# Kernel tuning notes

Measured on AMD Instinct MI355X. Metric: run time of the kernel, lower is better.

Reference implementation:

```python
import math
import jax, jax.numpy as jnp
import numpy as np

B, T, FDIM, ODIM = 16, 16, 64, 8
NQ, LAYERS, DEGREE = 10, 2, 3
NA = 4                      # ceil(log2(T))
TOT = NQ + NA               # 14 total wires
NROTS = 4 * NQ * LAYERS     # 80 params per timestep
QROTS = 4 * NQ              # 40 (qff circuit, 1 layer)
C64 = jnp.complex64


def ry_mat(t):
    c = jnp.cos(0.5 * t).astype(C64)
    s = jnp.sin(0.5 * t).astype(C64)
    return jnp.stack([jnp.stack([c, -s], -1), jnp.stack([s, c], -1)], -2)


def rz_mat(t):
    p = jnp.exp(-0.5j * t.astype(C64))
    q = jnp.exp(0.5j * t.astype(C64))
    z = jnp.zeros_like(p)
    return jnp.stack([jnp.stack([p, z], -1), jnp.stack([z, q], -1)], -2)


def crx_mat(t):
    c = jnp.cos(0.5 * t).astype(C64)
    s = (-1j) * jnp.sin(0.5 * t).astype(C64)
    z = jnp.zeros_like(c)
    o = jnp.ones_like(c)
    r0 = jnp.stack([o, z, z, z], -1)
    r1 = jnp.stack([z, o, z, z], -1)
    r2 = jnp.stack([z, z, c, s], -1)
    r3 = jnp.stack([z, z, s, c], -1)
    return jnp.stack([r0, r1, r2, r3], -2)


CNOT = jnp.array([[1, 0, 0, 0], [0, 1, 0, 0], [0, 0, 0, 1], [0, 0, 1, 0]], dtype=C64)


def apply_gate(state, U, wires):
    # state: (Be, 2,...,2) tensor; wire w lives on axis w+1. U: (2^k,2^k) or (Be,2^k,2^k)
    k = len(wires)
    axes = [w + 1 for w in wires]
    st = jnp.moveaxis(state, axes, list(range(1, k + 1)))
    shp = st.shape
    st = st.reshape(shp[0], 2 ** k, -1)
    eq = 'bij,bjr->bir' if U.ndim == 3 else 'ij,bjr->bir'
    st = jnp.einsum(eq, U, st).reshape(shp)
    return jnp.moveaxis(st, list(range(1, k + 1)), axes)


def sim14_seq(nq, layers):
    # gate sequence of Sim et al. circuit 14: RY ring, CRX ring, RY ring, CRX counter-ring
    seq, idx = [], 0
    for _ in range(layers):
        for i in range(nq):
            seq.append(('ry', (i,), idx)); idx += 1
        for i in range(nq - 1, -1, -1):
            seq.append(('crx', (i, (i + 1) % nq), idx)); idx += 1
        for i in range(nq):
            seq.append(('ry', (i,), idx)); idx += 1
        for i in [nq - 1] + list(range(nq - 1)):
            seq.append(('crx', (i, (i - 1) % nq), idx)); idx += 1
    return seq


def apply_sim14(state, params, layers, adjoint=False):
    seq = sim14_seq(NQ, layers)
    if adjoint:
        seq = seq[::-1]
    sign = -1.0 if adjoint else 1.0
    for kind, w, pidx in seq:
        th = sign * params[..., pidx]
        U = ry_mat(th) if kind == 'ry' else crx_mat(th)
        state = apply_gate(state, U, list(w))
    return state


def apply_prepare(state, prep_p, adjoint=False):
    # learnable PREPARE ansatz on ancilla wires NQ..NQ+NA-1 (n_prep_layers == NA)
    seq = []
    for ly in range(NA):
        for qi in range(NA):
            seq.append(('ry', NQ + qi, (ly, qi, 0)))
            seq.append(('rz', NQ + qi, (ly, qi, 1)))
        for i in range(NA - 1):
            seq.append(('cnot', (NQ + i, NQ + i + 1), None))
    if adjoint:
        seq = seq[::-1]
    sign = -1.0 if adjoint else 1.0
    for kind, w, pix in seq:
        if kind == 'cnot':
            state = apply_gate(state, CNOT, list(w))
        else:
            th = sign * prep_p[pix]
            U = ry_mat(th) if kind == 'ry' else rz_mat(th)
            state = apply_gate(state, U, [w])
    return state


def pcphase(state, phi):
    # PennyLane PCPhase(phi, dim=2^NQ, wires=anc+main): e^{+i phi} on ancilla==0 subspace, e^{-i phi} elsewhere
    st = state.reshape(B, 2 ** NQ, 2 ** NA)
    ph = jnp.exp(1j * phi.astype(C64))
    vec = jnp.where(jnp.arange(2 ** NA) == 0, ph, jnp.conj(ph))
    return (st * vec).reshape((B,) + (2,) * TOT)


def apply_select(state, ts_params, adjoint=False):
    # Select: apply sim14(ts_params[:, j]) on main wires when ancilla register == j
    # (T == 2^NA so there is no identity padding). Vectorized over batch x ancilla index.
    st = state.reshape(B, 2 ** NQ, 2 ** NA)
    st = jnp.moveaxis(st, 2, 1).reshape((B * T,) + (2,) * NQ)
    st = apply_sim14(st, ts_params.reshape(B * T, NROTS), LAYERS, adjoint)
    st = st.reshape(B, 2 ** NA, 2 ** NQ)
    return jnp.moveaxis(st, 1, 2).reshape((B,) + (2,) * TOT)


def expvals(state):
    # <X_i>, <Y_i>, <Z_i> on main wires, order X0..X9, Y0..Y9, Z0..Z9
    xs, ys, zs = [], [], []
    for i in range(NQ):
        s = jnp.moveaxis(state, i + 1, 1).reshape(B, 2, -1)
        s0, s1 = s[:, 0], s[:, 1]
        c = jnp.sum(jnp.conj(s0) * s1, axis=-1)
        xs.append(2.0 * jnp.real(c))
        ys.append(2.0 * jnp.imag(c))
        zs.append(jnp.sum(jnp.abs(s0) ** 2 - jnp.abs(s1) ** 2, axis=-1))
    return jnp.stack(xs + ys + zs, axis=1).astype(jnp.float32)  # (B, 3*NQ)


def make_pe():
    pos = np.arange(T, dtype=np.float32)[:, None]
    div = np.exp(np.arange(0, FDIM, 2, dtype=np.float32) * -(math.log(10000.0) / FDIM))
    pe = np.zeros((T, FDIM), np.float32)
    pe[:, 0::2] = np.sin(pos * div)
    pe[:, 1::2] = np.cos(pos * div[:FDIM // 2])
    return jnp.asarray(pe)


def setup_inputs():
    key = jax.random.key(0)
    ks = jax.random.split(key, 8)
    return {
        'x': jax.random.normal(ks[0], (B, FDIM, T), jnp.float32),
        'W_fp': jax.random.normal(ks[1], (NROTS, FDIM), jnp.float32) / math.sqrt(FDIM),
        'b_fp': jnp.zeros((NROTS,), jnp.float32),
        'prep_p': 0.1 * jax.random.normal(ks[2], (NA, NA, 2), jnp.float32),
        'sig_ang': 0.1 * jax.random.normal(ks[3], (DEGREE + 1,), jnp.float32),
        'qff_p': jax.random.uniform(ks[4], (QROTS,), jnp.float32),
        'W_out': jax.random.normal(ks[5], (ODIM, 3 * NQ), jnp.float32) / math.sqrt(3 * NQ),
        'b_out': jnp.zeros((ODIM,), jnp.float32),
    }


def reference(x, W_fp, b_fp, prep_p, sig_ang, qff_p, W_out, b_out):
    h = jnp.transpose(x, (0, 2, 1)) + make_pe()[None]          # (B, T, FDIM)
    ts = jax.nn.sigmoid(h @ W_fp.T + b_fp) * (2.0 * math.pi)    # (B, T, NROTS)
    # |0...0> on all 14 wires, batched
    psi = jnp.zeros((B, 2 ** TOT), C64).at[:, 0].set(1.0).reshape((B,) + (2,) * TOT)
    psi = pcphase(psi, sig_ang[0])
    for k in range(DEGREE):
        psi = apply_prepare(psi, prep_p, adjoint=False)
        psi = apply_select(psi, ts, adjoint=(k % 2 == 1))
        psi = apply_prepare(psi, prep_p, adjoint=True)
        psi = pcphase(psi, sig_ang[k + 1])
    psi = apply_sim14(psi, qff_p, layers=1, adjoint=False)      # QFF readout circuit
    exps = expvals(psi)                                         # (B, 30)
    return exps @ W_out.T + b_out                               # (B, ODIM)
```

## Files before the change

kernel.cpp:

```cpp
#include <hip/hip_runtime.h>
#include <math.h>
#include <utility>


typedef float v2f __attribute__((ext_vector_type(2)));

struct Gate { int ry; int tbit; int cbit; int pidx; };
struct GateTab { Gate g[40]; };

constexpr GateTab make_gates1() {
  GateTab tb{};
  int pos = 0, idx = 0;
  for (int i = 0; i < 10; ++i) { tb.g[pos] = Gate{1, 9 - i, -1, idx}; ++pos; ++idx; }
  for (int i = 9; i >= 0; --i) { tb.g[pos] = Gate{0, 9 - ((i + 1) % 10), 9 - i, idx}; ++pos; ++idx; }
  for (int i = 0; i < 10; ++i) { tb.g[pos] = Gate{1, 9 - i, -1, idx}; ++pos; ++idx; }
  for (int k = 0; k < 10; ++k) {
    int i = (k == 0) ? 9 : (k - 1);
    tb.g[pos] = Gate{0, 9 - ((i + 9) % 10), 9 - i, idx}; ++pos; ++idx;
  }
  return tb;
}
constexpr GateTab GTC = make_gates1();

__device__ __forceinline__ int insert_zero(int v, int p) {
  return ((v >> p) << (p + 1)) | (v & ((1 << p) - 1));
}
__device__ __forceinline__ float2 cmul(float2 A, float2 B) {
  return make_float2(A.x * B.x - A.y * B.y, A.x * B.y + A.y * B.x);
}
__device__ __forceinline__ float2 conj2(float2 A) { return make_float2(A.x, -A.y); }
__device__ __forceinline__ v2f vmk(float x, float y) { v2f r; r.x = x; r.y = y; return r; }

template<int XM>
__device__ __forceinline__ float lxor(float v) {
  if constexpr (XM == 1) {
    int r = __builtin_amdgcn_update_dpp(__float_as_int(v), __float_as_int(v),
                                        0xB1, 0xF, 0xF, true);
    return __int_as_float(r);
  } else if constexpr (XM == 2) {
    int r = __builtin_amdgcn_update_dpp(__float_as_int(v), __float_as_int(v),
                                        0x4E, 0xF, 0xF, true);
    return __int_as_float(r);
  } else if constexpr (XM == 8) {
    int r = __builtin_amdgcn_update_dpp(__float_as_int(v), __float_as_int(v),
                                        0x128, 0xF, 0xF, true);
    return __int_as_float(r);
  } else if constexpr (XM == 16) {
#if __has_builtin(__builtin_amdgcn_permlane16_swap)
    unsigned uv = __float_as_uint(v);
    auto r = __builtin_amdgcn_permlane16_swap(uv, uv, false, false);
    return __uint_as_float(r[0] ^ r[1] ^ uv);
#else
    return __shfl_xor(v, 16, 64);
#endif
  } else if constexpr (XM == 32) {
#if __has_builtin(__builtin_amdgcn_permlane32_swap)
    unsigned uv = __float_as_uint(v);
    auto r = __builtin_amdgcn_permlane32_swap(uv, uv, false, false);
    return __uint_as_float(r[0] ^ r[1] ^ uv);
#else
    return __shfl_xor(v, 32, 64);
#endif
  } else {
    return __shfl_xor(v, XM, 64);
  }
}
template<int XM>
__device__ __forceinline__ v2f lxor2(v2f v) {
  v2f r; r.x = lxor<XM>(v.x); r.y = lxor<XM>(v.y); return r;
}

__device__ __forceinline__ float wave_sum(float v) {
  v += lxor<1>(v);
  v += lxor<2>(v);
  v += lxor<4>(v);
  v += lxor<8>(v);
  v += lxor<16>(v);
  v += lxor<32>(v);
  return v;
}

struct alignas(128) GBar {
  unsigned cnt;
  unsigned gen;
  unsigned done;
  unsigned pad[29];
};
__device__ GBar g_gb[16];

__device__ __forceinline__ void group_barrier16(int b, int lane) {
  unsigned snap = __hip_atomic_load(&g_gb[b].gen, __ATOMIC_RELAXED, __HIP_MEMORY_SCOPE_AGENT);
  if (lane == 0) {
    unsigned old = __hip_atomic_fetch_add(&g_gb[b].cnt, 1u, __ATOMIC_ACQ_REL,
                                          __HIP_MEMORY_SCOPE_AGENT);
    if ((old & 15u) == 15u)
      __hip_atomic_store(&g_gb[b].gen, snap + 1u, __ATOMIC_RELEASE,
                         __HIP_MEMORY_SCOPE_AGENT);
  }
  while (__hip_atomic_load(&g_gb[b].gen, __ATOMIC_RELAXED, __HIP_MEMORY_SCOPE_AGENT) == snap)
    __builtin_amdgcn_s_sleep(1);
  (void)__hip_atomic_load(&g_gb[b].gen, __ATOMIC_ACQUIRE, __HIP_MEMORY_SCOPE_AGENT);
}

template<int P>
__device__ __forceinline__ void ry_gate(v2f (&a)[16], float c, float s, int lane) {
  if constexpr (P < 4) {
    constexpr int m = 1 << P;
#pragma unroll
    for (int r0 = 0; r0 < 16; ++r0) {
      if (!(r0 & m)) {
        int r1 = r0 | m;
        v2f a0 = a[r0], a1 = a[r1];
        a[r0] = c * a0 - s * a1;
        a[r1] = s * a0 + c * a1;
      }
    }
  } else {
    constexpr int xm = 1 << (P - 4);
    bool up = (lane >> (P - 4)) & 1;
    float sg = up ? s : -s;
#pragma unroll
    for (int r = 0; r < 16; ++r) {
      v2f wv = lxor2<xm>(a[r]);
      a[r] = c * a[r] + sg * wv;
    }
  }
}

template<int P, int Q>
__device__ __forceinline__ void crx_gate(v2f (&a)[16], float c, float s, int lane) {
  if constexpr (P < 4) {
    constexpr int m = 1 << P;
#pragma unroll
    for (int r0 = 0; r0 < 16; ++r0) {
      if (!(r0 & m)) {
        int r1 = r0 | m;
        bool act;
        if constexpr (Q < 4) act = (r0 >> Q) & 1;
        else act = (lane >> (Q - 4)) & 1;
        if (act) {
          v2f a0 = a[r0], a1 = a[r1];
          a[r0] = c * a0 + s * vmk(a1.y, -a1.x);
          a[r1] = c * a1 + s * vmk(a0.y, -a0.x);
        }
      }
    }
  } else {
    constexpr int xm = 1 << (P - 4);
#pragma unroll
    for (int r = 0; r < 16; ++r) {
      v2f wv = lxor2<xm>(a[r]);
      bool act;
      if constexpr (Q < 4) act = (r >> Q) & 1;
      else act = (lane >> (Q - 4)) & 1;
      if (act) a[r] = c * a[r] + s * vmk(wv.y, -wv.x);
    }
  }
}

template<bool ADJ, int G>
__device__ __forceinline__ void one_gate(v2f (&a)[16], const float2 (&sc)[40], int lane) {
  constexpr Gate g = GTC.g[ADJ ? (39 - G) : G];
  float2 scv = sc[g.pidx];
  float s = ADJ ? -scv.x : scv.x;
  float c = scv.y;
  if constexpr (g.ry != 0) ry_gate<g.tbit>(a, c, s, lane);
  else crx_gate<g.tbit, g.cbit>(a, c, s, lane);
}

template<bool ADJ, int... I>
__device__ __forceinline__ void run_layer_impl(v2f (&a)[16], const float2 (&sc)[40],
                                               int lane, std::integer_sequence<int, I...>) {
  (one_gate<ADJ, I>(a, sc, lane), ...);
}

template<bool ADJ>
__device__ __forceinline__ void run_layer(v2f (&a)[16], const float2* sc, int lane) {
  float2 rsc[40];
#pragma unroll
  for (int i = 0; i < 40; ++i) rsc[i] = sc[i];
  run_layer_impl<ADJ>(a, rsc, lane, std::make_integer_sequence<int, 40>{});
}

__global__ __launch_bounds__(256, 1) void k_fused(const float* __restrict__ x,
                                                  const float* __restrict__ W_fp,
                                                  const float* __restrict__ b_fp,
                                                  const float* __restrict__ prep,
                                                  const float* __restrict__ sig,
                                                  const float* __restrict__ qff,
                                                  const float* __restrict__ W_out,
                                                  const float* __restrict__ b_out,
                                                  float* __restrict__ out,
                                                  float4* __restrict__ part1,
                                                  float4* __restrict__ part2,
                                                  float* __restrict__ sv) {
  int blk = blockIdx.x;
  int b = blk >> 2, sub = blk & 3;
  int tid = threadIdx.x;
  int w = tid >> 6, lane = tid & 63;
  int aa = sub * 4 + w;

  __shared__ __align__(16) float h[4][64];
  __shared__ float2 scs[4][80];
  __shared__ float2 qscs[40];
  __shared__ float2 ps[32];
  __shared__ float2 es[4];
  __shared__ float2 u0s[16];
  __shared__ float4 R[2][512];

  if (sub == 0 && w == 0 && lane < 30) sv[b * 30 + lane] = 0.f;

  {
    int f = lane, k = f >> 1;
    float div = expf(-(float)(2 * k) * (logf(10000.f) / 64.f));
    float ang = (float)aa * div;
    float pe = (f & 1) ? cosf(ang) : sinf(ang);
    h[w][f] = x[(b * 64 + f) * 16 + aa] + pe;
  }
  if (w == 0) {
    if (lane < 32) {
      float s, c;
      sincosf(0.5f * prep[lane], &s, &c);
      ps[lane] = make_float2(s, c);
    } else if (lane < 36) {
      float s, c;
      sincosf(sig[lane - 32], &s, &c);
      es[lane - 32] = make_float2(c, s);
    }
  } else if (w == 1 && lane < 40) {
    float s, c;
    sincosf(0.5f * qff[lane], &s, &c);
    qscs[lane] = make_float2(s, c);
  }
  __syncthreads();

  if (w == 0) {
    float2 v[16];
#pragma unroll
    for (int i = 0; i < 16; ++i) v[i] = make_float2(i == 0 ? 1.f : 0.f, 0.f);
#pragma unroll 1
    for (int ly = 0; ly < 4; ++ly) {
#pragma unroll
      for (int qi = 0; qi < 4; ++qi) {
        int p = 3 - qi;
        float2 rc = ps[ly * 8 + qi * 2 + 0];
        {
          float s = rc.x, c = rc.y;
#pragma unroll
          for (int m = 0; m < 8; ++m) {
            int a0 = insert_zero(m, p), a1 = a0 | (1 << p);
            float2 t0 = v[a0], t1 = v[a1];
            v[a0] = make_float2(c * t0.x - s * t1.x, c * t0.y - s * t1.y);
            v[a1] = make_float2(s * t0.x + c * t1.x, s * t0.y + c * t1.y);
          }
        }
        rc = ps[ly * 8 + qi * 2 + 1];
        {
          float s = rc.x, c = rc.y;
#pragma unroll
          for (int m = 0; m < 8; ++m) {
            int a0 = insert_zero(m, p), a1 = a0 | (1 << p);
            float2 t0 = v[a0], t1 = v[a1];
            v[a0] = make_float2(c * t0.x + s * t0.y, c * t0.y - s * t0.x);
            v[a1] = make_float2(c * t1.x - s * t1.y, c * t1.y + s * t1.x);
          }
        }
      }
#pragma unroll
      for (int i = 0; i < 3; ++i) {
        int pc = 3 - i, pt = 2 - i;
#pragma unroll
        for (int m = 0; m < 4; ++m) {
          int mm = insert_zero(m, pt);
          mm = insert_zero(mm, pc);
          int a0 = mm | (1 << pc), a1 = a0 | (1 << pt);
          float2 t0 = v[a0], t1 = v[a1];
          v[a0] = t1; v[a1] = t0;
        }
      }
    }
    if (lane == 0) {
#pragma unroll
      for (int i = 0; i < 16; ++i) u0s[i] = v[i];
    }
  }

  {
    const float4* h4 = (const float4*)&h[w][0];
    for (int j = lane; j < 80; j += 64) {
      float acc = b_fp[j];
      const float4* w4 = (const float4*)(W_fp + j * 64);
#pragma unroll
      for (int k4 = 0; k4 < 16; ++k4) {
        float4 hh = h4[k4], ww = w4[k4];
        acc += hh.x * ww.x + hh.y * ww.y + hh.z * ww.z + hh.w * ww.w;
      }
      float sg = 1.f / (1.f + expf(-acc));
      float s, c;
      sincosf(sg * 3.14159265358979323846f, &s, &c);
      scs[w][j] = make_float2(s, c);
    }
  }
  __syncthreads();

  float2 u0aa = u0s[aa];
  float2 e0 = es[0], e1 = es[1], e2 = es[2];
  float2 m0  = cmul(u0aa, e0);
  float2 cu0 = conj2(u0aa);
  float2 ceA = conj2(e1);
  float2 wA  = make_float2(-2.f * e1.y * u0aa.y, 2.f * e1.y * u0aa.x);
  float2 ceB = conj2(e2);
  float2 wB  = make_float2(-2.f * e2.y * u0aa.y, 2.f * e2.y * u0aa.x);

  const float2* sc = &scs[w][0];
  v2f a[16];
#pragma unroll
  for (int r = 0; r < 16; ++r) a[r] = vmk(0.f, 0.f);
  if (lane == 0) a[0] = vmk(m0.x, m0.y);

#pragma unroll 1
  for (int ph = 0; ph < 7; ++ph) {
    if (ph == 2 || ph == 4) {
      float2 ce = (ph == 2) ? ceA : ceB;
      float2 wk = (ph == 2) ? wA : wB;
      float4* part = (ph == 2) ? part1 : part2;

      __syncthreads();
      if (w < 2) {
#pragma unroll
        for (int q = 0; q < 8; ++q) {
          float2 p0 = cmul(cu0, make_float2(a[2 * q].x, a[2 * q].y));
          float2 p1 = cmul(cu0, make_float2(a[2 * q + 1].x, a[2 * q + 1].y));
          R[w][q * 64 + lane] = make_float4(p0.x, p0.y, p1.x, p1.y);
        }
      }
      __syncthreads();
      if (w >= 2) {
#pragma unroll
        for (int q = 0; q < 8; ++q) {
          float4 v = R[w - 2][q * 64 + lane];
          float2 p0 = cmul(cu0, make_float2(a[2 * q].x, a[2 * q].y));
          float2 p1 = cmul(cu0, make_float2(a[2 * q + 1].x, a[2 * q + 1].y));
          R[w - 2][q * 64 + lane] =
              make_float4(v.x + p0.x, v.y + p0.y, v.z + p1.x, v.w + p1.y);
        }
      }
      __syncthreads();
#pragma unroll
      for (int qq = 0; qq < 2; ++qq) {
        int q = w * 2 + qq;
        float4 v0 = R[0][q * 64 + lane];
        float4 v1 = R[1][q * 64 + lane];
        part[(size_t)(b * 4 + sub) * 512 + q * 64 + lane] =
            make_float4(v0.x + v1.x, v0.y + v1.y, v0.z + v1.z, v0.w + v1.w);
      }
      group_barrier16(b, lane);

      float4 s4[8];
#pragma unroll
      for (int q = 0; q < 8; ++q) {
        float4 v0 = R[0][q * 64 + lane];
        float4 v1 = R[1][q * 64 + lane];
        s4[q] = make_float4(v0.x + v1.x, v0.y + v1.y, v0.z + v1.z, v0.w + v1.w);
      }
#pragma unroll 1
      for (int o = 1; o < 4; ++o) {
        int so = (sub + o) & 3;
        const float4* pp = part + (size_t)(b * 4 + so) * 512 + lane;
#pragma unroll
        for (int q = 0; q < 8; ++q) {
          float4 v = pp[q * 64];
          s4[q].x += v.x; s4[q].y += v.y; s4[q].z += v.z; s4[q].w += v.w;
        }
      }
#pragma unroll
      for (int q = 0; q < 8; ++q) {
        v2f a0 = a[2 * q], a1 = a[2 * q + 1];
        a[2 * q] = vmk(ce.x * a0.x - ce.y * a0.y + wk.x * s4[q].x - wk.y * s4[q].y,
                       ce.x * a0.y + ce.y * a0.x + wk.x * s4[q].y + wk.y * s4[q].x);
        a[2 * q + 1] = vmk(ce.x * a1.x - ce.y * a1.y + wk.x * s4[q].z - wk.y * s4[q].w,
                           ce.x * a1.y + ce.y * a1.x + wk.x * s4[q].w + wk.y * s4[q].z);
      }
    }
    const float2* scp;
    if (ph == 6) scp = &qscs[0];
    else scp = sc + ((ph == 1 || ph == 2 || ph == 5) ? 40 : 0);
    if (ph == 2 || ph == 3) run_layer<true>(a, scp, lane);
    else                    run_layer<false>(a, scp, lane);
  }

  {
    float obs[30];
#pragma unroll
    for (int p = 0; p <= 9; ++p) {
      int i = 9 - p;
      float cr = 0.f, ci = 0.f, zz = 0.f;
      if (p < 4) {
        int m = 1 << p;
#pragma unroll
        for (int r0 = 0; r0 < 16; ++r0) {
          if (!(r0 & m)) {
            v2f A0 = a[r0], A1 = a[r0 | m];
            cr += A0.x * A1.x + A0.y * A1.y;
            ci += A0.x * A1.y - A0.y * A1.x;
            zz += (A0.x * A0.x + A0.y * A0.y) - (A1.x * A1.x + A1.y * A1.y);
          }
        }
      } else {
        int xm = 1 << (p - 4);
        bool up = (lane >> (p - 4)) & 1;
#pragma unroll
        for (int r = 0; r < 16; ++r) {
          float wx = __shfl_xor(a[r].x, xm, 64);
          float wy = __shfl_xor(a[r].y, xm, 64);
          float n2 = a[r].x * a[r].x + a[r].y * a[r].y;
          if (!up) {
            cr += a[r].x * wx + a[r].y * wy;
            ci += a[r].x * wy - a[r].y * wx;
            zz += n2;
          } else {
            zz -= n2;
          }
        }
      }
      obs[i] = 2.f * cr;
      obs[10 + i] = 2.f * ci;
      obs[20 + i] = zz;
    }
#pragma unroll
    for (int j = 0; j < 30; ++j) obs[j] = wave_sum(obs[j]);

    float* Rf = (float*)R;
    __syncthreads();
    if (lane == 0) {
#pragma unroll
      for (int j = 0; j < 30; ++j) Rf[w * 30 + j] = obs[j];
    }
    __syncthreads();
    if (w == 0) {
      if (lane < 30) {
        float v = Rf[0 * 30 + lane] + Rf[1 * 30 + lane] +
                  Rf[2 * 30 + lane] + Rf[3 * 30 + lane];
        atomicAdd(&sv[b * 30 + lane], v);
      }
      int lastflag = 0;
      if (lane == 0) {
        unsigned old = __hip_atomic_fetch_add(&g_gb[b].done, 1u, __ATOMIC_ACQ_REL,
                                              __HIP_MEMORY_SCOPE_AGENT);
        lastflag = ((old & 3u) == 3u) ? 1 : 0;
      }
      lastflag = __shfl(lastflag, 0, 64);
      if (lastflag) {
        (void)__hip_atomic_load(&g_gb[b].done, __ATOMIC_ACQUIRE, __HIP_MEMORY_SCOPE_AGENT);
        if (lane < 8) {
          float acc = b_out[lane];
#pragma unroll
          for (int j = 0; j < 30; ++j) acc += W_out[lane * 30 + j] * sv[b * 30 + j];
          out[b * 8 + lane] = acc;
        }
      }
    }
  }
}

extern "C" void kernel_launch(void* const* d_in, const int* in_sizes, int n_in,
                              void* d_out, int out_size, void* d_ws, size_t ws_size,
                              hipStream_t stream) {
  const float* x     = (const float*)d_in[0];
  const float* W_fp  = (const float*)d_in[1];
  const float* b_fp  = (const float*)d_in[2];
  const float* prep  = (const float*)d_in[3];
  const float* sig   = (const float*)d_in[4];
  const float* qff   = (const float*)d_in[5];
  const float* W_out = (const float*)d_in[6];
  const float* b_out = (const float*)d_in[7];
  float* out = (float*)d_out;
  (void)in_sizes; (void)n_in; (void)out_size;

  char* ws = (char*)d_ws;
  const size_t SZ_PART = (size_t)64 * 512 * 16;
  float4* part1 = (float4*)ws;
  float4* part2 = (float4*)(ws + SZ_PART);
  float*  sv    = (float*)(ws + 2 * SZ_PART);
  (void)ws_size;

  k_fused<<<dim3(64), dim3(256), 0, stream>>>(x, W_fp, b_fp, prep, sig, qff,
                                              W_out, b_out, out, part1, part2, sv);
}
```

Before: 163.5 us.

## Make CRX gates branch-free, use fast intrinsics, and remap blocks across CUs

```diff
diff --git a/kernel.cpp b/kernel.cpp
--- a/kernel.cpp
+++ b/kernel.cpp
@@ -40,6 +40,9 @@
   } else if constexpr (XM == 2) {
     int r = __builtin_amdgcn_update_dpp(__float_as_int(v), __float_as_int(v),
                                         0x4E, 0xF, 0xF, true);
+    return __int_as_float(r);
+  } else if constexpr (XM == 4) {
+    int r = __builtin_amdgcn_ds_swizzle(__float_as_int(v), 0x101F);
     return __int_as_float(r);
   } else if constexpr (XM == 8) {
     int r = __builtin_amdgcn_update_dpp(__float_as_int(v), __float_as_int(v),
@@ -53,7 +56,7 @@
 #else
     return __shfl_xor(v, 16, 64);
 #endif
-  } else if constexpr (XM == 32) {
+  } else {
 #if __has_builtin(__builtin_amdgcn_permlane32_swap)
     unsigned uv = __float_as_uint(v);
     auto r = __builtin_amdgcn_permlane32_swap(uv, uv, false, false);
@@ -61,8 +64,6 @@
 #else
     return __shfl_xor(v, 32, 64);
 #endif
-  } else {
-    return __shfl_xor(v, XM, 64);
   }
 }
 template<int XM>
@@ -80,11 +81,11 @@
   return v;
 }
 
-struct alignas(128) GBar {
+struct alignas(256) GBar {
   unsigned cnt;
   unsigned gen;
   unsigned done;
-  unsigned pad[29];
+  unsigned pad[61];
 };
 __device__ GBar g_gb[16];
 
@@ -127,22 +128,20 @@
   }
 }
 
-template<int P, int Q>
-__device__ __forceinline__ void crx_gate(v2f (&a)[16], float c, float s, int lane) {
+__device__ __forceinline__ v2f crot(v2f v, float c, float s, v2f w) {
+  return c * v + s * vmk(w.y, -w.x);
+}
+template<int P>
+__device__ __forceinline__ void crx_body(v2f (&a)[16], float c, float s, int lane) {
   if constexpr (P < 4) {
     constexpr int m = 1 << P;
 #pragma unroll
     for (int r0 = 0; r0 < 16; ++r0) {
       if (!(r0 & m)) {
         int r1 = r0 | m;
-        bool act;
-        if constexpr (Q < 4) act = (r0 >> Q) & 1;
-        else act = (lane >> (Q - 4)) & 1;
-        if (act) {
-          v2f a0 = a[r0], a1 = a[r1];
-          a[r0] = c * a0 + s * vmk(a1.y, -a1.x);
-          a[r1] = c * a1 + s * vmk(a0.y, -a0.x);
-        }
+        v2f a0 = a[r0], a1 = a[r1];
+        a[r0] = crot(a0, c, s, a1);
+        a[r1] = crot(a1, c, s, a0);
       }
     }
   } else {
@@ -150,16 +149,45 @@
 #pragma unroll
     for (int r = 0; r < 16; ++r) {
       v2f wv = lxor2<xm>(a[r]);
-      bool act;
-      if constexpr (Q < 4) act = (r >> Q) & 1;
-      else act = (lane >> (Q - 4)) & 1;
-      if (act) a[r] = c * a[r] + s * vmk(wv.y, -wv.x);
+      a[r] = crot(a[r], c, s, wv);
+    }
+  }
+}
+
+template<int P, int Q>
+__device__ __forceinline__ void crx_gate(v2f (&a)[16], float c, float s, int lane) {
+  if constexpr (Q >= 4) {
+    bool act = (lane >> (Q - 4)) & 1;
+    float cm = act ? c : 1.f;
+    float sm = act ? s : 0.f;
+    crx_body<P>(a, cm, sm, lane);
+  } else {
+    if constexpr (P < 4) {
+      constexpr int m = 1 << P;
+#pragma unroll
+      for (int r0 = 0; r0 < 16; ++r0) {
+        if (!(r0 & m) && ((r0 >> Q) & 1)) {
+          int r1 = r0 | m;
+          v2f a0 = a[r0], a1 = a[r1];
+          a[r0] = crot(a0, c, s, a1);
+          a[r1] = crot(a1, c, s, a0);
+        }
+      }
+    } else {
+      constexpr int xm = 1 << (P - 4);
+#pragma unroll
+      for (int r = 0; r < 16; ++r) {
+        if ((r >> Q) & 1) {
+          v2f wv = lxor2<xm>(a[r]);
+          a[r] = crot(a[r], c, s, wv);
+        }
+      }
     }
   }
 }
 
 template<bool ADJ, int G>
-__device__ __forceinline__ void one_gate(v2f (&a)[16], const float2 (&sc)[40], int lane) {
+__device__ __forceinline__ void one_gate(v2f (&a)[16], const float2* sc, int lane) {
   constexpr Gate g = GTC.g[ADJ ? (39 - G) : G];
   float2 scv = sc[g.pidx];
   float s = ADJ ? -scv.x : scv.x;
@@ -169,17 +197,13 @@
 }
 
 template<bool ADJ, int... I>
-__device__ __forceinline__ void run_layer_impl(v2f (&a)[16], const float2 (&sc)[40],
+__device__ __forceinline__ void run_layer_impl(v2f (&a)[16], const float2* sc,
                                                int lane, std::integer_sequence<int, I...>) {
   (one_gate<ADJ, I>(a, sc, lane), ...);
 }
-
 template<bool ADJ>
 __device__ __forceinline__ void run_layer(v2f (&a)[16], const float2* sc, int lane) {
-  float2 rsc[40];
-#pragma unroll
-  for (int i = 0; i < 40; ++i) rsc[i] = sc[i];
-  run_layer_impl<ADJ>(a, rsc, lane, std::make_integer_sequence<int, 40>{});
+  run_layer_impl<ADJ>(a, sc, lane, std::make_integer_sequence<int, 40>{});
 }
 
 __global__ __launch_bounds__(256, 1) void k_fused(const float* __restrict__ x,
@@ -195,7 +219,7 @@
                                                   float4* __restrict__ part2,
                                                   float* __restrict__ sv) {
   int blk = blockIdx.x;
-  int b = blk >> 2, sub = blk & 3;
+  int b = blk & 15, sub = blk >> 4;
   int tid = threadIdx.x;
   int w = tid >> 6, lane = tid & 63;
   int aa = sub * 4 + w;
@@ -212,25 +236,27 @@
 
   {
     int f = lane, k = f >> 1;
-    float div = expf(-(float)(2 * k) * (logf(10000.f) / 64.f));
+    float div = __expf(-(float)(2 * k) * (logf(10000.f) / 64.f));
     float ang = (float)aa * div;
-    float pe = (f & 1) ? cosf(ang) : sinf(ang);
+    float sa, ca;
+    __sincosf(ang, &sa, &ca);
+    float pe = (f & 1) ? ca : sa;
     h[w][f] = x[(b * 64 + f) * 16 + aa] + pe;
   }
-  if (w == 0) {
+  if (w == 1) {
     if (lane < 32) {
-      float s, c;
-      sincosf(0.5f * prep[lane], &s, &c);
-      ps[lane] = make_float2(s, c);
+      float s, cc;
+      __sincosf(0.5f * prep[lane], &s, &cc);
+      ps[lane] = make_float2(s, cc);
     } else if (lane < 36) {
-      float s, c;
-      sincosf(sig[lane - 32], &s, &c);
-      es[lane - 32] = make_float2(c, s);
-    }
-  } else if (w == 1 && lane < 40) {
-    float s, c;
-    sincosf(0.5f * qff[lane], &s, &c);
-    qscs[lane] = make_float2(s, c);
+      float s, cc;
+      __sincosf(sig[lane - 32], &s, &cc);
+      es[lane - 32] = make_float2(cc, s);
+    }
+  } else if (w == 2 && lane < 40) {
+    float s, cc;
+    __sincosf(0.5f * qff[lane], &s, &cc);
+    qscs[lane] = make_float2(s, cc);
   }
   __syncthreads();
 
@@ -245,24 +271,24 @@
         int p = 3 - qi;
         float2 rc = ps[ly * 8 + qi * 2 + 0];
         {
-          float s = rc.x, c = rc.y;
+          float s = rc.x, cc = rc.y;
 #pragma unroll
           for (int m = 0; m < 8; ++m) {
             int a0 = insert_zero(m, p), a1 = a0 | (1 << p);
             float2 t0 = v[a0], t1 = v[a1];
-            v[a0] = make_float2(c * t0.x - s * t1.x, c * t0.y - s * t1.y);
-            v[a1] = make_float2(s * t0.x + c * t1.x, s * t0.y + c * t1.y);
+            v[a0] = make_float2(cc * t0.x - s * t1.x, cc * t0.y - s * t1.y);
+            v[a1] = make_float2(s * t0.x + cc * t1.x, s * t0.y + cc * t1.y);
           }
         }
         rc = ps[ly * 8 + qi * 2 + 1];
         {
-          float s = rc.x, c = rc.y;
+          float s = rc.x, cc = rc.y;
 #pragma unroll
           for (int m = 0; m < 8; ++m) {
             int a0 = insert_zero(m, p), a1 = a0 | (1 << p);
             float2 t0 = v[a0], t1 = v[a1];
-            v[a0] = make_float2(c * t0.x + s * t0.y, c * t0.y - s * t0.x);
-            v[a1] = make_float2(c * t1.x - s * t1.y, c * t1.y + s * t1.x);
+            v[a0] = make_float2(cc * t0.x + s * t0.y, cc * t0.y - s * t0.x);
+            v[a1] = make_float2(cc * t1.x - s * t1.y, cc * t1.y + s * t1.x);
           }
         }
       }
@@ -295,10 +321,10 @@
         float4 hh = h4[k4], ww = w4[k4];
         acc += hh.x * ww.x + hh.y * ww.y + hh.z * ww.z + hh.w * ww.w;
       }
-      float sg = 1.f / (1.f + expf(-acc));
-      float s, c;
-      sincosf(sg * 3.14159265358979323846f, &s, &c);
-      scs[w][j] = make_float2(s, c);
+      float sg = 1.f / (1.f + __expf(-acc));
+      float s, cc;
+      __sincosf(sg * 3.14159265358979323846f, &s, &cc);
+      scs[w][j] = make_float2(s, cc);
     }
   }
   __syncthreads();
@@ -363,7 +389,7 @@
         float4 v1 = R[1][q * 64 + lane];
         s4[q] = make_float4(v0.x + v1.x, v0.y + v1.y, v0.z + v1.z, v0.w + v1.w);
       }
-#pragma unroll 1
+#pragma unroll
       for (int o = 1; o < 4; ++o) {
         int so = (sub + o) & 3;
         const float4* pp = part + (size_t)(b * 4 + so) * 512 + lane;
```

After: 159.2 us. -2.7%, faster.
